# Performance work log

Measured on AMD Instinct MI355X. Metric: run time of the kernel, lower is better.

## Reference

```python
import jax, jax.numpy as jnp
import numpy as np

B, T, D, K = 8, 4096, 512, 4096


def setup_inputs() -> dict:
    key = jax.random.key(0)
    k1, k2 = jax.random.split(key)
    x = jax.random.normal(k1, (B, T, D), dtype=jnp.float32)
    embed = jax.random.normal(k2, (K, D), dtype=jnp.float32)
    return {"x": x, "embed": embed}


def reference(x, embed):
    # F.normalize(x, p=2, dim=-1) with eps clamp like torch (eps=1e-12)
    norm = jnp.sqrt(jnp.sum(x * x, axis=-1, keepdims=True))
    xn = x / jnp.maximum(norm, 1e-12)

    flat = xn.reshape(-1, D)  # [(B*T), D]
    x_sq = jnp.sum(flat * flat, axis=1, keepdims=True)           # [(B*T), 1]
    e_sq = jnp.sum(embed * embed, axis=1)[None, :]               # [1, K]
    dist = -(x_sq - 2.0 * (flat @ embed.T) + e_sq)               # [(B*T), K]
    embed_ind = jnp.argmax(dist, axis=-1).reshape(B, T)          # [B, T]

    # decode: embedding gather then 'b n d -> b d n'
    quantize = embed[embed_ind]                                  # [B, T, D]
    quantize = jnp.transpose(quantize, (0, 2, 1))                # [B, D, T]
    return embed_ind, quantize
```

## Files before the change

### kernel.cpp

```cpp
#include <hip/hip_runtime.h>
#include <math.h>

#define BB 8
#define TT 4096
#define DDIM 512
#define KK 4096
#define NN (BB*TT)
#define EPS 0.05f

typedef __attribute__((ext_vector_type(8))) short bf16x8;
typedef __attribute__((ext_vector_type(4))) float f32x4;

__device__ __forceinline__ void async16(void* lds, const void* g) {
  __builtin_amdgcn_global_load_lds((const __attribute__((address_space(1))) void*)g,
                                   (__attribute__((address_space(3))) void*)lds, 16, 0, 0);
}

__device__ __forceinline__ unsigned pk_bf16(float a, float b) {
  unsigned ua = __float_as_uint(a); ua += 0x7FFFu + ((ua >> 16) & 1u);
  unsigned ub = __float_as_uint(b); ub += 0x7FFFu + ((ub >> 16) & 1u);
  return (ua >> 16) | (ub & 0xFFFF0000u);
}

__global__ __launch_bounds__(256) void prep_kernel(const float* __restrict__ src,
                                                   short* __restrict__ dst16,
                                                   float* __restrict__ outv, int mode) {
  int r = blockIdx.x * 4 + (threadIdx.x >> 6);
  int lane = threadIdx.x & 63;
  const float4* row4 = (const float4*)(src + (size_t)r * DDIM);
  float4 v0 = row4[lane];
  float4 v1 = row4[lane + 64];
  uint2 p0, p1;
  p0.x = pk_bf16(v0.x, v0.y); p0.y = pk_bf16(v0.z, v0.w);
  p1.x = pk_bf16(v1.x, v1.y); p1.y = pk_bf16(v1.z, v1.w);
  *(uint2*)(dst16 + (size_t)r * DDIM + lane * 4) = p0;
  *(uint2*)(dst16 + (size_t)r * DDIM + 256 + lane * 4) = p1;
  float ss = v0.x*v0.x + v0.y*v0.y + v0.z*v0.z + v0.w*v0.w
           + v1.x*v1.x + v1.y*v1.y + v1.z*v1.z + v1.w*v1.w;
  #pragma unroll
  for (int off = 32; off; off >>= 1) ss += __shfl_down(ss, off);
  if (lane == 0) outv[r] = mode ? 2.0f / fmaxf(sqrtf(ss), 1e-12f) : ss;
}

__global__ __launch_bounds__(256, 2) void vq_mfma(const short* __restrict__ xb,
                                                  const short* __restrict__ eb,
                                                  const float* __restrict__ esq,
                                                  const float* __restrict__ inv2,
                                                  float4* __restrict__ top2) {
  __shared__ short As[128 * 64];
  __shared__ short Bs[128 * 64];
  __shared__ float rS1[2][128];
  __shared__ float rS2[2][128];
  __shared__ int   rI1[2][128];

  const int tid = threadIdx.x;
  const int lane = tid & 63;
  const int w = tid >> 6;
  const int wr = w >> 1, wc = w & 1;
  const int q = lane >> 4, c16 = lane & 15;

  const int mb = blockIdx.x & 255;
  const int kq = blockIdx.x >> 8;
  const int n0 = mb * 128;
  const int kbase = kq * 1024;

  const int srow = w * 32 + (lane >> 3);
  const int scol = ((lane & 7) ^ (lane >> 3)) * 8;
  const short* gA = xb + (size_t)(n0 + srow) * DDIM + scol;

  float s1[16], s2v[16];
  int   i1[16];
  #pragma unroll
  for (int s = 0; s < 16; ++s) { s1[s] = -3e38f; s2v[s] = -3e38f; i1[s] = 0; }

  float4 inv4[4];
  #pragma unroll
  for (int ti = 0; ti < 4; ++ti)
    inv4[ti] = *(const float4*)&inv2[n0 + wr * 64 + ti * 16 + q * 4];

  for (int c = 0; c < 8; ++c) {
    const int k0c = kbase + c * 128;
    const short* gB = eb + (size_t)(k0c + srow) * DDIM + scol;
    f32x4 acc[4][4];
    #pragma unroll
    for (int ti = 0; ti < 4; ++ti)
      #pragma unroll
      for (int tj = 0; tj < 4; ++tj) acc[ti][tj] = (f32x4){0.f, 0.f, 0.f, 0.f};

    for (int d0 = 0; d0 < DDIM; d0 += 64) {
      #pragma unroll
      for (int i = 0; i < 4; ++i) {
        async16(As + (w * 32 + i * 8) * 64, gA + (size_t)i * 8 * DDIM + d0);
        async16(Bs + (w * 32 + i * 8) * 64, gB + (size_t)i * 8 * DDIM + d0);
      }
      __syncthreads();
      #pragma unroll
      for (int ks = 0; ks < 2; ++ks) {
        const int ko = (((ks << 2) | q) ^ (lane & 7)) << 3;
        bf16x8 af[4], bf[4];
        #pragma unroll
        for (int ti = 0; ti < 4; ++ti)
          af[ti] = *(const bf16x8*)&As[(wr * 64 + ti * 16 + c16) * 64 + ko];
        #pragma unroll
        for (int tj = 0; tj < 4; ++tj)
          bf[tj] = *(const bf16x8*)&Bs[(wc * 64 + tj * 16 + c16) * 64 + ko];
        #pragma unroll
        for (int ti = 0; ti < 4; ++ti)
          #pragma unroll
          for (int tj = 0; tj < 4; ++tj)
            acc[ti][tj] = __builtin_amdgcn_mfma_f32_16x16x32_bf16(af[ti], bf[tj], acc[ti][tj], 0, 0, 0);
      }
      __syncthreads();
    }
    #pragma unroll
    for (int tj = 0; tj < 4; ++tj) {
      const int col = k0c + wc * 64 + tj * 16 + c16;
      const float nes = -esq[col];
      #pragma unroll
      for (int ti = 0; ti < 4; ++ti)
        #pragma unroll
        for (int r = 0; r < 4; ++r) {
          int slot = ti * 4 + r;
          float sc = fmaf(acc[ti][tj][r], inv4[ti][r], nes);
          float mn = fminf(sc, s1[slot]);
          s2v[slot] = fmaxf(s2v[slot], mn);
          if (sc > s1[slot]) { s1[slot] = sc; i1[slot] = col; }
        }
    }
  }

  #pragma unroll
  for (int slot = 0; slot < 16; ++slot) {
    float a1 = s1[slot], a2 = s2v[slot]; int ai = i1[slot];
    #pragma unroll
    for (int off = 1; off < 16; off <<= 1) {
      float b1 = __shfl_xor(a1, off);
      float b2 = __shfl_xor(a2, off);
      int   bi = __shfl_xor(ai, off);
      float mn = fminf(a1, b1);
      a2 = fmaxf(fmaxf(a2, b2), mn);
      if (b1 > a1 || (b1 == a1 && bi < ai)) { a1 = b1; ai = bi; }
    }
    if (c16 == 0) {
      int row = wr * 64 + (slot >> 2) * 16 + q * 4 + (slot & 3);
      rS1[wc][row] = a1; rS2[wc][row] = a2; rI1[wc][row] = ai;
    }
  }
  __syncthreads();
  if (tid < 128) {
    float a1 = rS1[0][tid], a2 = rS2[0][tid]; int ai = rI1[0][tid];
    float b1 = rS1[1][tid], b2 = rS2[1][tid]; int bi = rI1[1][tid];
    float mn = fminf(a1, b1);
    a2 = fmaxf(fmaxf(a2, b2), mn);
    if (b1 > a1 || (b1 == a1 && bi < ai)) { a1 = b1; ai = bi; }
    top2[(size_t)kq * NN + n0 + tid] = make_float4(a1, __int_as_float(ai), a2, 0.f);
  }
}

__global__ __launch_bounds__(256) void finalize_kernel(const float4* __restrict__ top2,
                                                       float* __restrict__ out_ind,
                                                       int* __restrict__ flags,
                                                       int* __restrict__ list,
                                                       int* __restrict__ cnt) {
  int row = blockIdx.x * 256 + threadIdx.x;
  float a1 = -3e38f, a2 = -3e38f; int ai = 0;
  #pragma unroll
  for (int kq = 0; kq < 4; ++kq) {
    float4 t = top2[(size_t)kq * NN + row];
    float b1 = t.x, b2 = t.z; int bi = __float_as_int(t.y);
    float mn = fminf(a1, b1);
    a2 = fmaxf(fmaxf(a2, b2), mn);
    if (b1 > a1 || (b1 == a1 && bi < ai)) { a1 = b1; ai = bi; }
  }
  out_ind[row] = (float)ai;
  if (a1 - a2 < EPS) {
    int p = atomicAdd(cnt, 1);
    list[p] = row;
    flags[row] = p + 1;
  } else {
    flags[row] = 0;
  }
}

__global__ __launch_bounds__(256) void cleanup_kernel(const float* __restrict__ x,
                                                      const float* __restrict__ embed,
                                                      const float* __restrict__ esq,
                                                      const float* __restrict__ inv2,
                                                      const int* __restrict__ list,
                                                      const int* __restrict__ cnt,
                                                      float2* __restrict__ exact) {
  __shared__ float xr[DDIM];
  __shared__ float red_s[4];
  __shared__ int   red_i[4];
  const int rs = blockIdx.x & 31, kc = blockIdx.x >> 5;
  const int tid = threadIdx.x;
  const int lane = tid & 63, wid = tid >> 6;
  const int n = *cnt;
  for (int ii = rs; ii < n; ii += 32) {
    const int row = list[ii];
    __syncthreads();
    if (tid < 128) *(float4*)&xr[tid * 4] = *(const float4*)&x[(size_t)row * DDIM + tid * 4];
    __syncthreads();
    const float iv = inv2[row];
    float bs = -3e38f; int bi = 0;
    for (int cc = 0; cc < 2; ++cc) {
      const int code = kc * 512 + cc * 256 + tid;
      const float4* er = (const float4*)&embed[(size_t)code * DDIM];
      float acc = 0.f;
      for (int d = 0; d < DDIM / 4; ++d) {
        float4 e4 = er[d];
        float4 x4 = *(const float4*)&xr[d * 4];
        acc += x4.x * e4.x + x4.y * e4.y + x4.z * e4.z + x4.w * e4.w;
      }
      float sc = fmaf(acc, iv, -esq[code]);
      if (sc > bs || (sc == bs && code < bi)) { bs = sc; bi = code; }
    }
    #pragma unroll
    for (int off = 1; off < 64; off <<= 1) {
      float b1 = __shfl_xor(bs, off);
      int   b2 = __shfl_xor(bi, off);
      if (b1 > bs || (b1 == bs && b2 < bi)) { bs = b1; bi = b2; }
    }
    if (lane == 0) { red_s[wid] = bs; red_i[wid] = bi; }
    __syncthreads();
    if (tid == 0) {
      for (int ww = 1; ww < 4; ++ww)
        if (red_s[ww] > red_s[0] || (red_s[ww] == red_s[0] && red_i[ww] < red_i[0])) {
          red_s[0] = red_s[ww]; red_i[0] = red_i[ww];
        }
      exact[(size_t)ii * 8 + kc] = make_float2(red_s[0], (float)red_i[0]);
    }
  }
}

__global__ __launch_bounds__(256) void gather_kernel(const float* __restrict__ embed,
                                                     const int* __restrict__ flags,
                                                     const float2* __restrict__ exact,
                                                     float* __restrict__ out_ind,
                                                     float* __restrict__ out_q) {
  __shared__ int lidx[64];
  __shared__ float trans[64 * 65];
  const int n0 = blockIdx.x * 64;
  const int tid = threadIdx.x;
  if (tid < 64) {
    const int row = n0 + tid;
    const int f = flags[row];
    int idx;
    if (f) {
      float bsv = -3e38f; int bi = 0;
      const float2* e8 = &exact[(size_t)(f - 1) * 8];
      #pragma unroll
      for (int k = 0; k < 8; ++k) {
        float2 t = e8[k];
        int ci = (int)t.y;
        if (t.x > bsv || (t.x == bsv && ci < bi)) { bsv = t.x; bi = ci; }
      }
      idx = bi;
      out_ind[row] = (float)idx;
    } else {
      idx = (int)out_ind[row];
    }
    lidx[tid] = idx;
  }
  __syncthreads();
  const int bb = n0 >> 12;
  const int t0 = n0 & (TT - 1);
  const int w = tid >> 6, lane = tid & 63;
  for (int d0 = 0; d0 < DDIM; d0 += 64) {
    if (d0) __syncthreads();
    #pragma unroll
    for (int qq = 0; qq < 16; ++qq) {
      int tt2 = w * 16 + qq;
      int e = lidx[tt2];
      trans[lane * 65 + tt2] = embed[(size_t)e * DDIM + d0 + lane];
    }
    __syncthreads();
    #pragma unroll
    for (int qq = 0; qq < 4; ++qq) {
      int dl = (tid >> 4) * 4 + qq;
      int t4 = (tid & 15) * 4;
      float4 o;
      o.x = trans[dl * 65 + t4 + 0];
      o.y = trans[dl * 65 + t4 + 1];
      o.z = trans[dl * 65 + t4 + 2];
      o.w = trans[dl * 65 + t4 + 3];
      *(float4*)&out_q[((size_t)bb * DDIM + d0 + dl) * TT + t0 + t4] = o;
    }
  }
}

extern "C" void kernel_launch(void* const* d_in, const int* in_sizes, int n_in,
                              void* d_out, int out_size, void* d_ws, size_t ws_size,
                              hipStream_t stream) {
  const float* x     = (const float*)d_in[0];
  const float* embed = (const float*)d_in[1];
  char* ws = (char*)d_ws;
  short* xb      = (short*)(ws);
  short* eb      = (short*)(ws + 33554432);
  float* esq     = (float*)(ws + 37748736);
  float* inv2    = (float*)(ws + 37765120);
  float4* top2   = (float4*)(ws + 37896192);
  int* list      = (int*)(ws + 39993344);
  int* flags     = (int*)(ws + 40124416);
  float2* exact  = (float2*)(ws + 40255488);
  int* cnt       = (int*)(ws + 42352640);

  float* out_ind = (float*)d_out;
  float* out_q   = out_ind + NN;

  prep_kernel<<<KK / 4, 256, 0, stream>>>(embed, eb, esq, 0);
  prep_kernel<<<NN / 4, 256, 0, stream>>>(x, xb, inv2, 1);
  hipMemsetAsync(cnt, 0, 4, stream);
  vq_mfma<<<1024, 256, 0, stream>>>(xb, eb, esq, inv2, top2);
  finalize_kernel<<<NN / 256, 256, 0, stream>>>(top2, out_ind, flags, list, cnt);
  cleanup_kernel<<<256, 256, 0, stream>>>(x, embed, esq, inv2, list, cnt, exact);
  gather_kernel<<<NN / 64, 256, 0, stream>>>(embed, flags, exact, out_ind, out_q);
}
```

Measured before the change: 327.4 us.

## Restructure VQ GEMM into 256x256 tiles with 4-stage async LDS pipeline

Rewrites the bf16 MFMA distance kernel to use 512-thread blocks computing 256x256 output tiles. Operands are streamed through a 4-buffer LDS ring with global_load_lds prefetch three steps ahead, fine-grained vmcnt waits and split barriers, so loads overlap the MFMA work. It also adds setprio around the MFMA bursts and stages inverse norms and codebook norms in LDS. The top-2 reduction is now done per 256-column chunk and merged through LDS instead of being kept in registers across chunks. The larger tile raises data reuse, but it also raises register pressure (128 accumulator floats per thread), and block-level parallelism is halved.

```diff
diff --git a/kernel.cpp b/kernel.cpp
--- a/kernel.cpp
+++ b/kernel.cpp
@@ -42,117 +42,169 @@
   if (lane == 0) outv[r] = mode ? 2.0f / fmaxf(sqrtf(ss), 1e-12f) : ss;
 }
 
-__global__ __launch_bounds__(256, 2) void vq_mfma(const short* __restrict__ xb,
+__global__ __launch_bounds__(512, 2) void vq_mfma(const short* __restrict__ xb,
                                                   const short* __restrict__ eb,
                                                   const float* __restrict__ esq,
                                                   const float* __restrict__ inv2,
                                                   float4* __restrict__ top2) {
-  __shared__ short As[128 * 64];
-  __shared__ short Bs[128 * 64];
-  __shared__ float rS1[2][128];
-  __shared__ float rS2[2][128];
-  __shared__ int   rI1[2][128];
+  __shared__ __attribute__((aligned(16))) short As[4 * 256 * 32];
+  __shared__ __attribute__((aligned(16))) short Bs[4 * 256 * 32];
+  __shared__ float rS1[4][256];
+  __shared__ float rS2[4][256];
+  __shared__ int   rI1[4][256];
+  __shared__ __attribute__((aligned(16))) float invLds[256];
+  __shared__ float esqLds[1024];
 
   const int tid = threadIdx.x;
   const int lane = tid & 63;
   const int w = tid >> 6;
-  const int wr = w >> 1, wc = w & 1;
+  const int wr = w >> 2;
+  const int wc = w & 3;
   const int q = lane >> 4, c16 = lane & 15;
 
-  const int mb = blockIdx.x & 255;
-  const int kq = blockIdx.x >> 8;
-  const int n0 = mb * 128;
+  const int mb = blockIdx.x >> 2;
+  const int kq = blockIdx.x & 3;
+  const int n0 = mb * 256;
   const int kbase = kq * 1024;
 
-  const int srow = w * 32 + (lane >> 3);
-  const int scol = ((lane & 7) ^ (lane >> 3)) * 8;
-  const short* gA = xb + (size_t)(n0 + srow) * DDIM + scol;
-
-  float s1[16], s2v[16];
-  int   i1[16];
-  #pragma unroll
-  for (int s = 0; s < 16; ++s) { s1[s] = -3e38f; s2v[s] = -3e38f; i1[s] = 0; }
-
-  float4 inv4[4];
-  #pragma unroll
-  for (int ti = 0; ti < 4; ++ti)
-    inv4[ti] = *(const float4*)&inv2[n0 + wr * 64 + ti * 16 + q * 4];
-
-  for (int c = 0; c < 8; ++c) {
-    const int k0c = kbase + c * 128;
-    const short* gB = eb + (size_t)(k0c + srow) * DDIM + scol;
-    f32x4 acc[4][4];
-    #pragma unroll
-    for (int ti = 0; ti < 4; ++ti)
-      #pragma unroll
-      for (int tj = 0; tj < 4; ++tj) acc[ti][tj] = (f32x4){0.f, 0.f, 0.f, 0.f};
-
-    for (int d0 = 0; d0 < DDIM; d0 += 64) {
-      #pragma unroll
-      for (int i = 0; i < 4; ++i) {
-        async16(As + (w * 32 + i * 8) * 64, gA + (size_t)i * 8 * DDIM + d0);
-        async16(Bs + (w * 32 + i * 8) * 64, gB + (size_t)i * 8 * DDIM + d0);
-      }
-      __syncthreads();
-      #pragma unroll
-      for (int ks = 0; ks < 2; ++ks) {
-        const int ko = (((ks << 2) | q) ^ (lane & 7)) << 3;
-        bf16x8 af[4], bf[4];
-        #pragma unroll
-        for (int ti = 0; ti < 4; ++ti)
-          af[ti] = *(const bf16x8*)&As[(wr * 64 + ti * 16 + c16) * 64 + ko];
+  if (tid < 256) invLds[tid] = inv2[n0 + tid];
+  esqLds[tid]       = -esq[kbase + tid];
+  esqLds[tid + 512] = -esq[kbase + 512 + tid];
+  __syncthreads();
+
+  const int sxq = (lane & 7) ^ (lane >> 3);
+  const int sb  = sxq >> 2;
+  const int sq  = sxq & 3;
+  const int srow = w * 16 + (lane >> 3) * 2 + sb;
+  const short* gA = xb + (size_t)(n0 + srow) * DDIM + sq * 8;
+  const short* gB = eb + (size_t)(kbase + srow) * DDIM + sq * 8;
+  short* sA = As + w * 512;
+  short* sB = Bs + w * 512;
+
+  const int sigma = (((c16 & 1) * 4 + q) ^ (c16 >> 1));
+  const int aoff = wr * 4096 + (c16 >> 1) * 64 + sigma * 8;
+  const int boff = wc * 2048 + (c16 >> 1) * 64 + sigma * 8;
+
+#define STAGE_A(u3) do { int t_ = (u3) & 15, b_ = (u3) & 3;              \
+    const short* g_ = gA + t_ * 32;                                      \
+    async16(sA + b_ * 8192,        g_);                                  \
+    async16(sA + b_ * 8192 + 4096, g_ + 128 * DDIM); } while (0)
+#define STAGE_B(u3) do { int c_ = (u3) >> 4, t_ = (u3) & 15, b_ = (u3) & 3; \
+    const short* g_ = gB + (size_t)c_ * (256 * DDIM) + t_ * 32;          \
+    async16(sB + b_ * 8192,        g_);                                  \
+    async16(sB + b_ * 8192 + 4096, g_ + 128 * DDIM); } while (0)
+
+  STAGE_A(0); STAGE_B(0);
+  STAGE_A(1); STAGE_B(1);
+  STAGE_A(2); STAGE_B(2);
+  asm volatile("s_waitcnt vmcnt(8)" ::: "memory");
+  asm volatile("s_barrier" ::: "memory");
+
+  for (int c = 0; c < 4; ++c) {
+    f32x4 acc[8][4];
+    #pragma unroll
+    for (int ti = 0; ti < 8; ++ti)
+      #pragma unroll
+      for (int tj = 0; tj < 4; ++tj)
+        acc[ti][tj] = (f32x4){0.f, 0.f, 0.f, 0.f};
+
+    #pragma unroll 4
+    for (int t = 0; t < 16; ++t) {
+      const int u = c * 16 + t;
+      const short* Ab = As + (u & 3) * 8192;
+      const short* Bb = Bs + (u & 3) * 8192;
+      bf16x8 af0[4], bfr[4];
+      #pragma unroll
+      for (int ti = 0; ti < 4; ++ti)
+        af0[ti] = *(const bf16x8*)(Ab + ti * 512 + aoff);
+      #pragma unroll
+      for (int tj = 0; tj < 4; ++tj)
+        bfr[tj] = *(const bf16x8*)(Bb + tj * 512 + boff);
+      if (u < 61) STAGE_A(u + 3);
+      asm volatile("s_barrier" ::: "memory");
+      __builtin_amdgcn_s_setprio(1);
+      #pragma unroll
+      for (int ti = 0; ti < 4; ++ti)
         #pragma unroll
         for (int tj = 0; tj < 4; ++tj)
-          bf[tj] = *(const bf16x8*)&Bs[(wc * 64 + tj * 16 + c16) * 64 + ko];
-        #pragma unroll
-        for (int ti = 0; ti < 4; ++ti)
-          #pragma unroll
-          for (int tj = 0; tj < 4; ++tj)
-            acc[ti][tj] = __builtin_amdgcn_mfma_f32_16x16x32_bf16(af[ti], bf[tj], acc[ti][tj], 0, 0, 0);
-      }
-      __syncthreads();
-    }
-    #pragma unroll
-    for (int tj = 0; tj < 4; ++tj) {
-      const int col = k0c + wc * 64 + tj * 16 + c16;
-      const float nes = -esq[col];
+          acc[ti][tj] = __builtin_amdgcn_mfma_f32_16x16x32_bf16(af0[ti], bfr[tj], acc[ti][tj], 0, 0, 0);
+      __builtin_amdgcn_s_setprio(0);
+      asm volatile("s_barrier" ::: "memory");
+      bf16x8 af1[4];
+      #pragma unroll
+      for (int ti = 0; ti < 4; ++ti)
+        af1[ti] = *(const bf16x8*)(Ab + (ti + 4) * 512 + aoff);
+      if (u < 61) STAGE_B(u + 3);
+      if (u < 61)       asm volatile("s_waitcnt vmcnt(8)" ::: "memory");
+      else if (u == 61) asm volatile("s_waitcnt vmcnt(4)" ::: "memory");
+      else if (u == 62) asm volatile("s_waitcnt vmcnt(0)" ::: "memory");
+      asm volatile("s_barrier" ::: "memory");
+      __builtin_amdgcn_s_setprio(1);
       #pragma unroll
       for (int ti = 0; ti < 4; ++ti)
         #pragma unroll
-        for (int r = 0; r < 4; ++r) {
-          int slot = ti * 4 + r;
-          float sc = fmaf(acc[ti][tj][r], inv4[ti][r], nes);
-          float mn = fminf(sc, s1[slot]);
-          s2v[slot] = fmaxf(s2v[slot], mn);
-          if (sc > s1[slot]) { s1[slot] = sc; i1[slot] = col; }
+        for (int tj = 0; tj < 4; ++tj)
+          acc[ti + 4][tj] = __builtin_amdgcn_mfma_f32_16x16x32_bf16(af1[ti], bfr[tj], acc[ti + 4][tj], 0, 0, 0);
+      __builtin_amdgcn_s_setprio(0);
+      asm volatile("s_barrier" ::: "memory");
+    }
+
+    float nes[4];
+    #pragma unroll
+    for (int tj = 0; tj < 4; ++tj)
+      nes[tj] = esqLds[c * 256 + wc * 64 + tj * 16 + c16];
+    const int colbase = kbase + c * 256 + wc * 64 + c16;
+    #pragma unroll
+    for (int ti = 0; ti < 8; ++ti) {
+      f32x4 iv4 = *(const f32x4*)&invLds[wr * 128 + ti * 16 + q * 4];
+      #pragma unroll
+      for (int r = 0; r < 4; ++r) {
+        const float iv = iv4[r];
+        float a1 = -3e38f, a2 = -3e38f; int ai = 0;
+        #pragma unroll
+        for (int tj = 0; tj < 4; ++tj) {
+          float sc = fmaf(acc[ti][tj][r], iv, nes[tj]);
+          float mn = fminf(sc, a1);
+          a2 = fmaxf(a2, mn);
+          if (sc > a1) { a1 = sc; ai = colbase + tj * 16; }
         }
-    }
-  }
-
-  #pragma unroll
-  for (int slot = 0; slot < 16; ++slot) {
-    float a1 = s1[slot], a2 = s2v[slot]; int ai = i1[slot];
-    #pragma unroll
-    for (int off = 1; off < 16; off <<= 1) {
-      float b1 = __shfl_xor(a1, off);
-      float b2 = __shfl_xor(a2, off);
-      int   bi = __shfl_xor(ai, off);
+        #pragma unroll
+        for (int off = 1; off < 16; off <<= 1) {
+          float b1 = __shfl_xor(a1, off);
+          float b2 = __shfl_xor(a2, off);
+          int   bi = __shfl_xor(ai, off);
+          float mn = fminf(a1, b1);
+          a2 = fmaxf(fmaxf(a2, b2), mn);
+          if (b1 > a1) { a1 = b1; ai = bi; }
+        }
+        if (c16 == 0) {
+          const int row = wr * 128 + ti * 16 + q * 4 + r;
+          if (c == 0) {
+            rS1[wc][row] = a1; rS2[wc][row] = a2; rI1[wc][row] = ai;
+          } else {
+            float o1 = rS1[wc][row], o2 = rS2[wc][row]; int oi = rI1[wc][row];
+            float mn = fminf(a1, o1);
+            o2 = fmaxf(fmaxf(a2, o2), mn);
+            if (a1 > o1) { o1 = a1; oi = ai; }
+            rS1[wc][row] = o1; rS2[wc][row] = o2; rI1[wc][row] = oi;
+          }
+        }
+      }
+    }
+  }
+#undef STAGE_A
+#undef STAGE_B
+
+  __syncthreads();
+  if (tid < 256) {
+    float a1 = rS1[0][tid], a2 = rS2[0][tid]; int ai = rI1[0][tid];
+    #pragma unroll
+    for (int g = 1; g < 4; ++g) {
+      float b1 = rS1[g][tid], b2 = rS2[g][tid]; int bi = rI1[g][tid];
       float mn = fminf(a1, b1);
       a2 = fmaxf(fmaxf(a2, b2), mn);
       if (b1 > a1 || (b1 == a1 && bi < ai)) { a1 = b1; ai = bi; }
     }
-    if (c16 == 0) {
-      int row = wr * 64 + (slot >> 2) * 16 + q * 4 + (slot & 3);
-      rS1[wc][row] = a1; rS2[wc][row] = a2; rI1[wc][row] = ai;
-    }
-  }
-  __syncthreads();
-  if (tid < 128) {
-    float a1 = rS1[0][tid], a2 = rS2[0][tid]; int ai = rI1[0][tid];
-    float b1 = rS1[1][tid], b2 = rS2[1][tid]; int bi = rI1[1][tid];
-    float mn = fminf(a1, b1);
-    a2 = fmaxf(fmaxf(a2, b2), mn);
-    if (b1 > a1 || (b1 == a1 && bi < ai)) { a1 = b1; ai = bi; }
     top2[(size_t)kq * NN + n0 + tid] = make_float4(a1, __int_as_float(ai), a2, 0.f);
   }
 }
@@ -311,7 +363,7 @@
   prep_kernel<<<KK / 4, 256, 0, stream>>>(embed, eb, esq, 0);
   prep_kernel<<<NN / 4, 256, 0, stream>>>(x, xb, inv2, 1);
   hipMemsetAsync(cnt, 0, 4, stream);
-  vq_mfma<<<1024, 256, 0, stream>>>(xb, eb, esq, inv2, top2);
+  vq_mfma<<<512, 512, 0, stream>>>(xb, eb, esq, inv2, top2);
   finalize_kernel<<<NN / 256, 256, 0, stream>>>(top2, out_ind, flags, list, cnt);
   cleanup_kernel<<<256, 256, 0, stream>>>(x, embed, esq, inv2, list, cnt, exact);
   gather_kernel<<<NN / 64, 256, 0, stream>>>(embed, flags, exact, out_ind, out_q);
```

Result: slower. 395.6 us (+20.8%).

## Keep full X tile resident in LDS, stream double-buffered codebook, fuse finalize

Applied to the files above, without the earlier changes.

The MFMA kernel now loads each block's whole 128x512 bf16 X tile into LDS once and streams codebook chunks of 256 codes x 32 dims through a double-buffered LDS area, so each step needs one barrier and the next chunk's load overlaps compute. Blocks grow to 512 threads (8 waves, a 2x4 layout) and cover all 4096 codes, so the K split and the separate finalize kernel are dropped, and the top-2 merge and ambiguity flagging happen in-kernel. s_setprio is wrapped around the MFMA burst. The change removes X reloads and the top2 round trip, but leaves only 256 blocks on the GPU and uses about 160KB of LDS per block, which limits occupancy.

```diff
diff --git a/kernel.cpp b/kernel.cpp
--- a/kernel.cpp
+++ b/kernel.cpp
@@ -42,93 +42,114 @@
   if (lane == 0) outv[r] = mode ? 2.0f / fmaxf(sqrtf(ss), 1e-12f) : ss;
 }
 
-__global__ __launch_bounds__(256, 2) void vq_mfma(const short* __restrict__ xb,
+__global__ __launch_bounds__(512, 2) void vq_mfma(const short* __restrict__ xb,
                                                   const short* __restrict__ eb,
                                                   const float* __restrict__ esq,
                                                   const float* __restrict__ inv2,
-                                                  float4* __restrict__ top2) {
-  __shared__ short As[128 * 64];
-  __shared__ short Bs[128 * 64];
-  __shared__ float rS1[2][128];
-  __shared__ float rS2[2][128];
-  __shared__ int   rI1[2][128];
+                                                  float* __restrict__ out_ind,
+                                                  int* __restrict__ flags,
+                                                  int* __restrict__ list,
+                                                  int* __restrict__ cnt) {
+  __shared__ __attribute__((aligned(16))) short As[128 * 512];
+  __shared__ __attribute__((aligned(16))) short Bs[2 * 256 * 32];
 
   const int tid = threadIdx.x;
   const int lane = tid & 63;
   const int w = tid >> 6;
-  const int wr = w >> 1, wc = w & 1;
+  const int wr = w >> 2;
+  const int wc = w & 3;
   const int q = lane >> 4, c16 = lane & 15;
-
-  const int mb = blockIdx.x & 255;
-  const int kq = blockIdx.x >> 8;
-  const int n0 = mb * 128;
-  const int kbase = kq * 1024;
-
-  const int srow = w * 32 + (lane >> 3);
-  const int scol = ((lane & 7) ^ (lane >> 3)) * 8;
-  const short* gA = xb + (size_t)(n0 + srow) * DDIM + scol;
+  const int n0 = blockIdx.x * 128;
+
+  #pragma unroll
+  for (int j = 0; j < 16; ++j)
+    async16(As + (j * 8 + w) * 512,
+            xb + (size_t)(n0 + j * 8 + w) * 512 + (lane ^ w) * 8);
+
+  const int x = (lane & 7) ^ (lane >> 3);
+  const int scode = w * 16 + (lane >> 3) * 2 + (x >> 2);
+  const short* gB = eb + (size_t)scode * 512 + (x & 3) * 8;
+  short* sB0 = Bs + w * 512;
+  async16(sB0,        gB);
+  async16(sB0 + 4096, gB + 128 * 512);
+
+  const int sigB8 = ((((c16 & 1) << 2) | q) ^ ((c16 >> 1) & 7)) * 8;
+  const int brow0 = (wc * 32 + (c16 >> 1)) * 64 + sigB8;
+  const int arow0 = (wr * 64 + c16) * 512;
+
+  f32x4 iv4[4];
+  #pragma unroll
+  for (int ti = 0; ti < 4; ++ti)
+    iv4[ti] = *(const f32x4*)&inv2[n0 + wr * 64 + ti * 16 + q * 4];
 
   float s1[16], s2v[16];
   int   i1[16];
   #pragma unroll
   for (int s = 0; s < 16; ++s) { s1[s] = -3e38f; s2v[s] = -3e38f; i1[s] = 0; }
 
-  float4 inv4[4];
-  #pragma unroll
-  for (int ti = 0; ti < 4; ++ti)
-    inv4[ti] = *(const float4*)&inv2[n0 + wr * 64 + ti * 16 + q * 4];
-
-  for (int c = 0; c < 8; ++c) {
-    const int k0c = kbase + c * 128;
-    const short* gB = eb + (size_t)(k0c + srow) * DDIM + scol;
+  __syncthreads();
+
+  for (int ct = 0; ct < 16; ++ct) {
+    float nes[4];
+    #pragma unroll
+    for (int tj = 0; tj < 4; ++tj)
+      nes[tj] = -esq[ct * 256 + wc * 64 + tj * 16 + c16];
     f32x4 acc[4][4];
     #pragma unroll
     for (int ti = 0; ti < 4; ++ti)
       #pragma unroll
       for (int tj = 0; tj < 4; ++tj) acc[ti][tj] = (f32x4){0.f, 0.f, 0.f, 0.f};
 
-    for (int d0 = 0; d0 < DDIM; d0 += 64) {
-      #pragma unroll
-      for (int i = 0; i < 4; ++i) {
-        async16(As + (w * 32 + i * 8) * 64, gA + (size_t)i * 8 * DDIM + d0);
-        async16(Bs + (w * 32 + i * 8) * 64, gB + (size_t)i * 8 * DDIM + d0);
+    #pragma unroll 2
+    for (int s = 0; s < 16; ++s) {
+      const int g = ct * 16 + s;
+      if (g < 255) {
+        const int gn = g + 1;
+        const short* src = gB + (size_t)(gn >> 4) * (256 * 512) + (gn & 15) * 32;
+        short* dst = Bs + ((gn & 1) << 13) + w * 512;
+        async16(dst,        src);
+        async16(dst + 4096, src + 128 * 512);
       }
-      __syncthreads();
-      #pragma unroll
-      for (int ks = 0; ks < 2; ++ks) {
-        const int ko = (((ks << 2) | q) ^ (lane & 7)) << 3;
-        bf16x8 af[4], bf[4];
-        #pragma unroll
-        for (int ti = 0; ti < 4; ++ti)
-          af[ti] = *(const bf16x8*)&As[(wr * 64 + ti * 16 + c16) * 64 + ko];
+      const short* Ap = As + arow0;
+      const short* Bp = Bs + ((g & 1) << 13) + brow0;
+      const int ach = ((s * 4 + q) ^ (c16 & 7)) * 8;
+      bf16x8 af[4], bf[4];
+      #pragma unroll
+      for (int ti = 0; ti < 4; ++ti)
+        af[ti] = *(const bf16x8*)(Ap + ti * 8192 + ach);
+      #pragma unroll
+      for (int tj = 0; tj < 4; ++tj)
+        bf[tj] = *(const bf16x8*)(Bp + tj * 512);
+      __builtin_amdgcn_s_setprio(1);
+      #pragma unroll
+      for (int ti = 0; ti < 4; ++ti)
         #pragma unroll
         for (int tj = 0; tj < 4; ++tj)
-          bf[tj] = *(const bf16x8*)&Bs[(wc * 64 + tj * 16 + c16) * 64 + ko];
+          acc[ti][tj] = __builtin_amdgcn_mfma_f32_16x16x32_bf16(af[ti], bf[tj], acc[ti][tj], 0, 0, 0);
+      __builtin_amdgcn_s_setprio(0);
+      __syncthreads();
+    }
+
+    const int colbase = ct * 256 + wc * 64 + c16;
+    #pragma unroll
+    for (int ti = 0; ti < 4; ++ti)
+      #pragma unroll
+      for (int r = 0; r < 4; ++r) {
+        const int slot = ti * 4 + r;
+        const float iv = iv4[ti][r];
         #pragma unroll
-        for (int ti = 0; ti < 4; ++ti)
-          #pragma unroll
-          for (int tj = 0; tj < 4; ++tj)
-            acc[ti][tj] = __builtin_amdgcn_mfma_f32_16x16x32_bf16(af[ti], bf[tj], acc[ti][tj], 0, 0, 0);
-      }
-      __syncthreads();
-    }
-    #pragma unroll
-    for (int tj = 0; tj < 4; ++tj) {
-      const int col = k0c + wc * 64 + tj * 16 + c16;
-      const float nes = -esq[col];
-      #pragma unroll
-      for (int ti = 0; ti < 4; ++ti)
-        #pragma unroll
-        for (int r = 0; r < 4; ++r) {
-          int slot = ti * 4 + r;
-          float sc = fmaf(acc[ti][tj][r], inv4[ti][r], nes);
+        for (int tj = 0; tj < 4; ++tj) {
+          float sc = fmaf(acc[ti][tj][r], iv, nes[tj]);
           float mn = fminf(sc, s1[slot]);
           s2v[slot] = fmaxf(s2v[slot], mn);
-          if (sc > s1[slot]) { s1[slot] = sc; i1[slot] = col; }
+          if (sc > s1[slot]) { s1[slot] = sc; i1[slot] = colbase + tj * 16; }
         }
-    }
-  }
-
+      }
+  }
+
+  float* rS1 = (float*)Bs;
+  float* rS2 = rS1 + 512;
+  int*   rI1 = (int*)(rS2 + 512);
   #pragma unroll
   for (int slot = 0; slot < 16; ++slot) {
     float a1 = s1[slot], a2 = s2v[slot]; int ai = i1[slot];
@@ -143,42 +164,28 @@
     }
     if (c16 == 0) {
       int row = wr * 64 + (slot >> 2) * 16 + q * 4 + (slot & 3);
-      rS1[wc][row] = a1; rS2[wc][row] = a2; rI1[wc][row] = ai;
+      rS1[wc * 128 + row] = a1; rS2[wc * 128 + row] = a2; rI1[wc * 128 + row] = ai;
     }
   }
   __syncthreads();
   if (tid < 128) {
-    float a1 = rS1[0][tid], a2 = rS2[0][tid]; int ai = rI1[0][tid];
-    float b1 = rS1[1][tid], b2 = rS2[1][tid]; int bi = rI1[1][tid];
-    float mn = fminf(a1, b1);
-    a2 = fmaxf(fmaxf(a2, b2), mn);
-    if (b1 > a1 || (b1 == a1 && bi < ai)) { a1 = b1; ai = bi; }
-    top2[(size_t)kq * NN + n0 + tid] = make_float4(a1, __int_as_float(ai), a2, 0.f);
-  }
-}
-
-__global__ __launch_bounds__(256) void finalize_kernel(const float4* __restrict__ top2,
-                                                       float* __restrict__ out_ind,
-                                                       int* __restrict__ flags,
-                                                       int* __restrict__ list,
-                                                       int* __restrict__ cnt) {
-  int row = blockIdx.x * 256 + threadIdx.x;
-  float a1 = -3e38f, a2 = -3e38f; int ai = 0;
-  #pragma unroll
-  for (int kq = 0; kq < 4; ++kq) {
-    float4 t = top2[(size_t)kq * NN + row];
-    float b1 = t.x, b2 = t.z; int bi = __float_as_int(t.y);
-    float mn = fminf(a1, b1);
-    a2 = fmaxf(fmaxf(a2, b2), mn);
-    if (b1 > a1 || (b1 == a1 && bi < ai)) { a1 = b1; ai = bi; }
-  }
-  out_ind[row] = (float)ai;
-  if (a1 - a2 < EPS) {
-    int p = atomicAdd(cnt, 1);
-    list[p] = row;
-    flags[row] = p + 1;
-  } else {
-    flags[row] = 0;
+    float a1 = rS1[tid], a2 = rS2[tid]; int ai = rI1[tid];
+    #pragma unroll
+    for (int gq = 1; gq < 4; ++gq) {
+      float b1 = rS1[gq * 128 + tid], b2 = rS2[gq * 128 + tid]; int bi = rI1[gq * 128 + tid];
+      float mn = fminf(a1, b1);
+      a2 = fmaxf(fmaxf(a2, b2), mn);
+      if (b1 > a1 || (b1 == a1 && bi < ai)) { a1 = b1; ai = bi; }
+    }
+    const int row = n0 + tid;
+    out_ind[row] = (float)ai;
+    if (a1 - a2 < EPS) {
+      int p = atomicAdd(cnt, 1);
+      list[p] = row;
+      flags[row] = p + 1;
+    } else {
+      flags[row] = 0;
+    }
   }
 }
 
@@ -299,7 +306,6 @@
   short* eb      = (short*)(ws + 33554432);
   float* esq     = (float*)(ws + 37748736);
   float* inv2    = (float*)(ws + 37765120);
-  float4* top2   = (float4*)(ws + 37896192);
   int* list      = (int*)(ws + 39993344);
   int* flags     = (int*)(ws + 40124416);
   float2* exact  = (float2*)(ws + 40255488);
@@ -311,8 +317,7 @@
   prep_kernel<<<KK / 4, 256, 0, stream>>>(embed, eb, esq, 0);
   prep_kernel<<<NN / 4, 256, 0, stream>>>(x, xb, inv2, 1);
   hipMemsetAsync(cnt, 0, 4, stream);
-  vq_mfma<<<1024, 256, 0, stream>>>(xb, eb, esq, inv2, top2);
-  finalize_kernel<<<NN / 256, 256, 0, stream>>>(top2, out_ind, flags, list, cnt);
+  vq_mfma<<<256, 512, 0, stream>>>(xb, eb, esq, inv2, out_ind, flags, list, cnt);
   cleanup_kernel<<<256, 256, 0, stream>>>(x, embed, esq, inv2, list, cnt, exact);
   gather_kernel<<<NN / 64, 256, 0, stream>>>(embed, flags, exact, out_ind, out_q);
 }
```

New measurement: 317.8 us. 1.03x faster.
